# Kernel optimization log

Measured on AMD Instinct MI355X. Metric: run time of the kernel, lower is better.

The kernel has to match this reference:

```python
import jax, jax.numpy as jnp
import numpy as np

B, T_TEXT, T_AUDIO, D = 16, 512, 4096, 256
TEMPERATURE = 10.0


def setup_inputs() -> dict:
    key = jax.random.key(0)
    k1, k2 = jax.random.split(key)
    hidden_state = jax.random.normal(k1, (B, D, T_TEXT), dtype=jnp.float32)
    # monotone token centers in [0, T_AUDIO)
    centers = jnp.sort(
        jax.random.uniform(k2, (B, T_TEXT), dtype=jnp.float32, minval=0.0, maxval=float(T_AUDIO)),
        axis=-1,
    )
    # audio frame timestamps 0..A-1, shared across batch
    audio_timestamps = jnp.broadcast_to(
        jnp.arange(T_AUDIO, dtype=jnp.float32), (B, T_AUDIO)
    )
    return {
        "hidden_state": hidden_state,
        "centers": centers,
        "audio_timestamps": audio_timestamps,
    }


def reference(hidden_state, centers, audio_timestamps):
    # interpolation_weights: squared-distance score, temperature-scaled softmax over tokens
    # centers: [B, T], audio_timestamps: [B, A] -> diffs: [B, A, T]
    diffs = centers[:, None, :] - audio_timestamps[:, :, None]
    logits = (-(TEMPERATURE ** -2)) * jnp.square(diffs)  # [B, A, T]
    weights = jax.nn.softmax(logits, axis=-1)            # softmax over token dim
    # audio_aligned_representation: matmul + sum reduction, fused into one einsum
    # hidden_state: [B, D, T]; contract T with weights, then sum over audio axis A
    out = jnp.einsum("bdt,bat->bd", hidden_state, weights)
    return out
```

## Files before the change

### kernel.cpp

```cpp
#include <hip/hip_runtime.h>

#define B_ 16
#define T_ 512
#define A_ 4096
#define D_ 256
#define NEG_SCALE2 (-0.01f * 1.4426950408889634f)
#define CHUNK 256
#define RADIUS 96.0f

__global__ __launch_bounds__(1024) void k_aligner(const float* __restrict__ centers,
                                                  const float* __restrict__ ats,
                                                  const float* __restrict__ hidden,
                                                  float* __restrict__ out) {
    __shared__ float  sc[T_];
    __shared__ float2 ai[CHUNK];
    __shared__ float  wl[T_];

    const int tid = threadIdx.x;
    const int b  = blockIdx.y;
    const int a0 = blockIdx.x * CHUNK;

    float c = 0.f;
    if (tid < T_) {
        c = centers[b * T_ + tid];
        sc[tid] = c;
        wl[tid] = 0.f;
    }
    if (tid < CHUNK)
        ai[tid] = make_float2(ats[b * A_ + a0 + tid], 0.f);
    __syncthreads();

    const float lov = ai[0].x - RADIUS;
    const float hiv = ai[CHUNK - 1].x + RADIUS;
    const int tlo = __syncthreads_count(tid < T_ && c < lov);
    const int thi = T_ - __syncthreads_count(tid < T_ && c > hiv);

    const int f = tid >> 2;
    const int q = tid & 3;

    const int t0 = min(tlo & ~3, T_ - 64);
    const float* hrow = hidden + (size_t)(b * D_ + f) * T_;
    const float4* hp4 = (const float4*)(hrow + t0) + q * 4;
    const float4 hf0 = hp4[0], hf1 = hp4[1], hf2 = hp4[2], hf3 = hp4[3];

    const float myts = ai[f].x;
    float s0 = 0.f, s1 = 0.f;
    int t = tlo + q;
    for (; t + 4 < thi; t += 8) {
        float d0 = sc[t] - myts;
        float d1 = sc[t + 4] - myts;
        s0 += __builtin_exp2f(NEG_SCALE2 * d0 * d0);
        s1 += __builtin_exp2f(NEG_SCALE2 * d1 * d1);
    }
    if (t < thi) {
        float d0 = sc[t] - myts;
        s0 += __builtin_exp2f(NEG_SCALE2 * d0 * d0);
    }
    float s = s0 + s1;
    s += __shfl_xor(s, 1, 64);
    s += __shfl_xor(s, 2, 64);
    if (q == 0) ai[f].y = 1.0f / fmaxf(s, 1e-37f);
    __syncthreads();

    for (int base = tlo; base < thi; base += 64) {
        int tt = base + (tid >> 4);
        if (tt < thi) {
            float cc = sc[tt];
            float w0 = 0.f, w1 = 0.f;
            #pragma unroll
            for (int k = (tid & 15); k < CHUNK; k += 32) {
                float2 p = ai[k];
                float dp = cc - p.x;
                w0 += __builtin_exp2f(NEG_SCALE2 * dp * dp) * p.y;
                float2 qq = ai[k + 16];
                float dq = cc - qq.x;
                w1 += __builtin_exp2f(NEG_SCALE2 * dq * dq) * qq.y;
            }
            float w = w0 + w1;
            w += __shfl_xor(w, 1, 64);
            w += __shfl_xor(w, 2, 64);
            w += __shfl_xor(w, 4, 64);
            w += __shfl_xor(w, 8, 64);
            if ((tid & 15) == 0) wl[tt] = w;
        }
    }
    __syncthreads();

    const float4* wl4 = (const float4*)wl;
    const int wbase = (t0 >> 2) + q * 4;
    float accA = 0.f, accB = 0.f;
    {
        float4 w0 = wl4[wbase + 0], w1 = wl4[wbase + 1];
        float4 w2 = wl4[wbase + 2], w3 = wl4[wbase + 3];
        accA += hf0.x * w0.x + hf0.y * w0.y + hf0.z * w0.z + hf0.w * w0.w;
        accB += hf1.x * w1.x + hf1.y * w1.y + hf1.z * w1.z + hf1.w * w1.w;
        accA += hf2.x * w2.x + hf2.y * w2.y + hf2.z * w2.z + hf2.w * w2.w;
        accB += hf3.x * w3.x + hf3.y * w3.y + hf3.z * w3.z + hf3.w * w3.w;
    }
    for (int tt = t0 + 64 + q; tt < thi; tt += 4)
        accA += hrow[tt] * wl[tt];

    float acc = accA + accB;
    acc += __shfl_xor(acc, 1, 64);
    acc += __shfl_xor(acc, 2, 64);
    if (q == 0) atomicAdd(&out[b * D_ + f], acc);
}

extern "C" void kernel_launch(void* const* d_in, const int* in_sizes, int n_in,
                              void* d_out, int out_size, void* d_ws, size_t ws_size,
                              hipStream_t stream) {
    const float* hidden  = (const float*)d_in[0];
    const float* centers = (const float*)d_in[1];
    const float* ats     = (const float*)d_in[2];
    float* out  = (float*)d_out;

    k_aligner<<<dim3(A_ / CHUNK, B_), 1024, 0, stream>>>(centers, ats, hidden, out);
}
```

Baseline: 67.99 us.

## Split hidden-row reduction across two blocks per audio chunk

```diff
diff --git a/kernel.cpp b/kernel.cpp
--- a/kernel.cpp
+++ b/kernel.cpp
@@ -8,17 +8,19 @@
 #define CHUNK 256
 #define RADIUS 96.0f
 
-__global__ __launch_bounds__(1024) void k_aligner(const float* __restrict__ centers,
-                                                  const float* __restrict__ ats,
-                                                  const float* __restrict__ hidden,
-                                                  float* __restrict__ out) {
+__global__ __launch_bounds__(1024, 8) void k_aligner(const float* __restrict__ centers,
+                                                     const float* __restrict__ ats,
+                                                     const float* __restrict__ hidden,
+                                                     float* __restrict__ out) {
     __shared__ float  sc[T_];
     __shared__ float2 ai[CHUNK];
     __shared__ float  wl[T_];
 
-    const int tid = threadIdx.x;
-    const int b  = blockIdx.y;
-    const int a0 = blockIdx.x * CHUNK;
+    const int tid  = threadIdx.x;
+    const int b    = blockIdx.y;
+    const int cx   = blockIdx.x >> 1;
+    const int half = blockIdx.x & 1;
+    const int a0   = cx * CHUNK;
 
     float c = 0.f;
     if (tid < T_) {
@@ -35,14 +37,15 @@
     const int tlo = __syncthreads_count(tid < T_ && c < lov);
     const int thi = T_ - __syncthreads_count(tid < T_ && c > hiv);
 
+    const int t0 = min(tlo & ~3, T_ - 64);
+    const int r  = half * 128 + (tid >> 3);
+    const int e  = tid & 7;
+    const float* hrow = hidden + (size_t)(b * D_ + r) * T_;
+    const float4* hp4 = (const float4*)(hrow + t0) + e * 2;
+    const float4 hf0 = hp4[0], hf1 = hp4[1];
+
     const int f = tid >> 2;
     const int q = tid & 3;
-
-    const int t0 = min(tlo & ~3, T_ - 64);
-    const float* hrow = hidden + (size_t)(b * D_ + f) * T_;
-    const float4* hp4 = (const float4*)(hrow + t0) + q * 4;
-    const float4 hf0 = hp4[0], hf1 = hp4[1], hf2 = hp4[2], hf3 = hp4[3];
-
     const float myts = ai[f].x;
     float s0 = 0.f, s1 = 0.f;
     int t = tlo + q;
@@ -87,23 +90,21 @@
     __syncthreads();
 
     const float4* wl4 = (const float4*)wl;
-    const int wbase = (t0 >> 2) + q * 4;
-    float accA = 0.f, accB = 0.f;
+    const int wbase = (t0 >> 2) + e * 2;
+    float accA, accB;
     {
-        float4 w0 = wl4[wbase + 0], w1 = wl4[wbase + 1];
-        float4 w2 = wl4[wbase + 2], w3 = wl4[wbase + 3];
-        accA += hf0.x * w0.x + hf0.y * w0.y + hf0.z * w0.z + hf0.w * w0.w;
-        accB += hf1.x * w1.x + hf1.y * w1.y + hf1.z * w1.z + hf1.w * w1.w;
-        accA += hf2.x * w2.x + hf2.y * w2.y + hf2.z * w2.z + hf2.w * w2.w;
-        accB += hf3.x * w3.x + hf3.y * w3.y + hf3.z * w3.z + hf3.w * w3.w;
+        float4 w0 = wl4[wbase], w1 = wl4[wbase + 1];
+        accA = hf0.x * w0.x + hf0.y * w0.y + hf0.z * w0.z + hf0.w * w0.w;
+        accB = hf1.x * w1.x + hf1.y * w1.y + hf1.z * w1.z + hf1.w * w1.w;
     }
-    for (int tt = t0 + 64 + q; tt < thi; tt += 4)
+    for (int tt = t0 + 64 + e; tt < thi; tt += 8)
         accA += hrow[tt] * wl[tt];
 
     float acc = accA + accB;
     acc += __shfl_xor(acc, 1, 64);
     acc += __shfl_xor(acc, 2, 64);
-    if (q == 0) atomicAdd(&out[b * D_ + f], acc);
+    acc += __shfl_xor(acc, 4, 64);
+    if (e == 0) atomicAdd(&out[b * D_ + r], acc);
 }
 
 extern "C" void kernel_launch(void* const* d_in, const int* in_sizes, int n_in,
@@ -114,5 +115,5 @@
     const float* ats     = (const float*)d_in[2];
     float* out  = (float*)d_out;
 
-    k_aligner<<<dim3(A_ / CHUNK, B_), 1024, 0, stream>>>(centers, ats, hidden, out);
+    k_aligner<<<dim3(2 * (A_ / CHUNK), B_), 1024, 0, stream>>>(centers, ats, hidden, out);
 }
```

Measured after the change: 70.00 us. 3.0% more time.
